# Kernel tuning notes

Measured on AMD Instinct MI355X. Metric: run time of the kernel, lower is better.

Reference implementation:

```python
import jax, jax.numpy as jnp
import numpy as np

DT, TAU_S, TAU_M = 1.0, 4.0, 20.0
ALPHA = float(np.exp(-DT / TAU_S))   # synaptic current decay
BETA = float(np.exp(-DT / TAU_M))    # membrane potential decay
THRESH = 1.0
STEPS, BATCH, D1, D2 = 128, 256, 1024, 1024


def setup_inputs() -> dict:
    key = jax.random.key(0)
    k1, k2 = jax.random.split(key)
    inp = jax.random.uniform(k1, (STEPS, BATCH, D1), dtype=jnp.float32)
    # kaiming_normal_ on (d2, d1): std = sqrt(2 / fan_in), mu = 1.0
    weight = jax.random.normal(k2, (D2, D1), dtype=jnp.float32) * np.sqrt(2.0 / D1)
    return {"input": inp, "weight": weight}


def reference(input, weight):
    steps, batch = input.shape[0], input.shape[1]
    d2 = weight.shape[0]
    # Step i uses input[i-1]; precompute all linear projections at once.
    lin = jnp.einsum('tbi,oi->tbo', input[:-1], weight)  # [steps-1, B, d2]

    def step(carry, cur):
        syn, mem = carry
        # snntorch Synaptic, reset_mechanism='zero': reset from PREVIOUS mem
        reset = (mem > THRESH).astype(mem.dtype)
        syn = ALPHA * syn + cur
        mem = (BETA * mem + syn) * (1.0 - reset)
        spk = (mem > THRESH).astype(mem.dtype)
        return (syn, mem), (spk, mem, syn)

    init = (jnp.zeros((batch, d2), input.dtype), jnp.zeros((batch, d2), input.dtype))
    _, (spk, V, I) = jax.lax.scan(step, init, lin)
    z = jnp.zeros((1, batch, d2), input.dtype)  # step 0 stays zero
    output = jnp.concatenate([z, spk], axis=0)
    V = jnp.concatenate([z, V], axis=0)
    I = jnp.concatenate([z, I], axis=0)
    return output, V, I
```

## Files before the change

kernel.cpp:

```cpp
#include <hip/hip_runtime.h>
#include <hip/hip_fp16.h>


#define STEPS 128
#define BATCH 256
#define DIN   1024
#define DOUT  1024

#define ALPHA 0.7788007830714049f
#define BETA  0.9512294245007140f

constexpr int    GM      = (STEPS - 1) * BATCH;
constexpr size_t PLANE   = (size_t)BATCH * DOUT;
constexpr size_t W_ELEMS = (size_t)DOUT * DIN;

typedef __attribute__((ext_vector_type(8))) _Float16 half8;
typedef __attribute__((ext_vector_type(4))) float float4v;

__global__ __launch_bounds__(256)
void split_kernel(const float* __restrict__ x,
                  unsigned short* __restrict__ hi,
                  unsigned short* __restrict__ lo)
{
    const size_t i = (size_t)blockIdx.x * 256 + threadIdx.x;
    const float4 v = reinterpret_cast<const float4*>(x)[i];
    float f[4] = {v.x, v.y, v.z, v.w};
    unsigned short hb[4], lb[4];
#pragma unroll
    for (int j = 0; j < 4; ++j) {
        _Float16 h = (_Float16)f[j];
        _Float16 l = (_Float16)(f[j] - (float)h);
        hb[j] = *reinterpret_cast<unsigned short*>(&h);
        lb[j] = *reinterpret_cast<unsigned short*>(&l);
    }
    ushort4 hv = {hb[0], hb[1], hb[2], hb[3]};
    ushort4 lv = {lb[0], lb[1], lb[2], lb[3]};
    reinterpret_cast<ushort4*>(hi)[i] = hv;
    reinterpret_cast<ushort4*>(lo)[i] = lv;
}

__device__ __forceinline__ void load16(const unsigned short* g, unsigned short* l)
{
    __builtin_amdgcn_global_load_lds(
        (const __attribute__((address_space(1))) void*)g,
        (__attribute__((address_space(3))) void*)l, 16, 0, 0);
}

__device__ __forceinline__ half8 ldsr(unsigned addr)
{
    half8 r;
    asm volatile("ds_read_b128 %0, %1" : "=v"(r) : "v"(addr) : "memory");
    return r;
}

#define PHASE_PRE() do {                                        \
    __builtin_amdgcn_s_barrier();                               \
    asm volatile("s_waitcnt lgkmcnt(0)" ::: "memory");          \
    __builtin_amdgcn_sched_barrier(0);                          \
    __builtin_amdgcn_s_setprio(1);                              \
} while (0)

#define PHASE_POST() do {                                       \
    __builtin_amdgcn_s_setprio(0);                              \
    __builtin_amdgcn_sched_barrier(0);                          \
    __builtin_amdgcn_s_barrier();                               \
} while (0)

#define MFMA_BLK(MB, BV)                                        \
    _Pragma("unroll")                                           \
    for (int mm = 0; mm < 4; ++mm)                              \
        _Pragma("unroll")                                       \
        for (int nn = 0; nn < 4; ++nn)                          \
            acc[(MB) + mm][nn] = __builtin_amdgcn_mfma_f32_16x16x32_f16( \
                ah[(MB) + mm], BV[nn], acc[(MB) + mm][nn], 0, 0, 0)

__global__ __launch_bounds__(512, 2)
void gemm_kernel(const float* __restrict__ Af,
                 const unsigned short* __restrict__ Wh,
                 const unsigned short* __restrict__ Wl,
                 float* __restrict__ C)
{
    __shared__ __align__(16) unsigned short smem[65536];

    const int lin = blockIdx.x;
    const int xcd = lin & 7, slot = lin >> 3;
    const int mp  = xcd * 16 + (slot >> 2);
    const int nt  = slot & 3;
    if (mp >= GM / 256) return;
    const int m0 = mp * 256;
    const int n0 = nt * 256;

    const int t = threadIdx.x;
    const int w = t >> 6, l = t & 63;
    const int wr = w >> 2, wc = w & 3;
    const int lr = l & 15, q = l >> 4;

    const int swz = q ^ ((l >> 1) & 3);

    const unsigned rdA = (unsigned)((wr * 128 + lr) * 64 + swz * 16);
    const unsigned rdB = (unsigned)(32768 + (wc * 64 + lr) * 64 + swz * 16);

    const int srow = l >> 2;
    const int sgE  = ((l & 3) ^ ((l >> 3) & 3)) * 8;

    const size_t fA0 = (size_t)(m0 + w * 32 +      srow) * DIN + sgE;
    const size_t fA1 = (size_t)(m0 + w * 32 + 16 + srow) * DIN + sgE;
    const size_t sB0 = (size_t)(n0 + w * 32 +      srow) * DIN + sgE;
    const size_t sB1 = (size_t)(n0 + w * 32 + 16 + srow) * DIN + sgE;

    const unsigned dstA = (unsigned)(w * 1024 + l * 8);

    auto STAGE_W = [&](int ks) {
        const int kk = (ks & 31) << 5;
        unsigned short* d = smem + ((ks & 1) << 15) + w * 1024;
        load16(Wh + sB0 + kk, d + 16384);
        load16(Wh + sB1 + kk, d + 16896);
        load16(Wl + sB0 + kk, d + 24576);
        load16(Wl + sB1 + kk, d + 25088);
    };

    auto WRITE_A = [&](float4 x, float4 y, unsigned short* ds, unsigned off) {
        float f[8] = {x.x, x.y, x.z, x.w, y.x, y.y, y.z, y.w};
        half8 h, lo8;
#pragma unroll
        for (int j = 0; j < 8; ++j) {
            _Float16 hh = (_Float16)f[j];
            h[j]   = hh;
            lo8[j] = (_Float16)(f[j] - (float)hh);
        }
        *reinterpret_cast<half8*>(ds + dstA + off)        = h;
        *reinterpret_cast<half8*>(ds + dstA + off + 8192) = lo8;
    };

    float4v acc[8][4];
#pragma unroll
    for (int m = 0; m < 8; ++m)
#pragma unroll
        for (int n = 0; n < 4; ++n)
            acc[m][n] = (float4v){0.f, 0.f, 0.f, 0.f};

    {
        float4 a0 = *reinterpret_cast<const float4*>(Af + fA0);
        float4 a1 = *reinterpret_cast<const float4*>(Af + fA0 + 4);
        float4 a2 = *reinterpret_cast<const float4*>(Af + fA1);
        float4 a3 = *reinterpret_cast<const float4*>(Af + fA1 + 4);
        STAGE_W(0);
        unsigned short* ds = smem;
        WRITE_A(a0, a1, ds, 0);
        WRITE_A(a2, a3, ds, 512);
        asm volatile("s_waitcnt vmcnt(0) lgkmcnt(0)" ::: "memory");
        __builtin_amdgcn_s_barrier();
    }

    for (int kt = 0; kt < 32; ++kt) {
        const unsigned sb = (unsigned)((kt & 1) << 16);
        const int kn = ((kt + 1) & 31) << 5;
        half8 ah[8], bh[4], bl[4];

        float4 a0 = *reinterpret_cast<const float4*>(Af + fA0 + kn);
        float4 a1 = *reinterpret_cast<const float4*>(Af + fA0 + kn + 4);
        float4 a2 = *reinterpret_cast<const float4*>(Af + fA1 + kn);
        float4 a3 = *reinterpret_cast<const float4*>(Af + fA1 + kn + 4);
#pragma unroll
        for (int m = 0; m < 4; ++m) ah[m] = ldsr(sb + rdA + m * 1024);
#pragma unroll
        for (int n = 0; n < 4; ++n) bh[n] = ldsr(sb + rdB + n * 1024);
        PHASE_PRE();  MFMA_BLK(0, bh);  PHASE_POST();

#pragma unroll
        for (int m = 4; m < 8; ++m) ah[m] = ldsr(sb + rdA + m * 1024);
        PHASE_PRE();  MFMA_BLK(4, bh);  PHASE_POST();

#pragma unroll
        for (int n = 0; n < 4; ++n) bl[n] = ldsr(sb + rdB + 16384 + n * 1024);
        STAGE_W((kt + 1) & 31);
        PHASE_PRE();  MFMA_BLK(0, bl);  PHASE_POST();

#pragma unroll
        for (int m = 0; m < 4; ++m) ah[m] = ldsr(sb + rdA + 16384 + m * 1024);
        PHASE_PRE();  MFMA_BLK(4, bl);  PHASE_POST();

#pragma unroll
        for (int m = 4; m < 8; ++m) ah[m] = ldsr(sb + rdA + 16384 + m * 1024);
        PHASE_PRE();  MFMA_BLK(0, bh);  PHASE_POST();

        PHASE_PRE();  MFMA_BLK(4, bh);
        __builtin_amdgcn_s_setprio(0);
        __builtin_amdgcn_sched_barrier(0);
        {
            unsigned short* ds = smem + (((kt + 1) & 1) << 15);
            WRITE_A(a0, a1, ds, 0);
            WRITE_A(a2, a3, ds, 512);
        }
        asm volatile("s_waitcnt vmcnt(0) lgkmcnt(0)" ::: "memory");
        __builtin_amdgcn_s_barrier();
    }

    const int mw = m0 + wr * 128 + q * 4;
    const int nw = n0 + wc * 64 + lr;
#pragma unroll
    for (int m = 0; m < 8; ++m)
#pragma unroll
        for (int n = 0; n < 4; ++n)
#pragma unroll
            for (int rg = 0; rg < 4; ++rg)
                C[(size_t)(mw + m * 16 + rg) * DOUT + (nw + n * 16)] = acc[m][n][rg];
}

__global__ __launch_bounds__(256)
void scan_kernel(float* __restrict__ out)
{
    const int idx = blockIdx.x * 256 + threadIdx.x;
    float* o0 = out;
    float* o1 = out + STEPS * PLANE;
    float* o2 = out + 2 * STEPS * PLANE;

    __builtin_nontemporal_store(0.0f, &o0[idx]);
    __builtin_nontemporal_store(0.0f, &o1[idx]);
    __builtin_nontemporal_store(0.0f, &o2[idx]);

    float n1 = o2[idx + PLANE];
    float n2 = o2[idx + 2 * PLANE];
    float n3 = o2[idx + 3 * PLANE];

    float syn = 0.0f, mem = 0.0f;
    size_t off = idx;
    for (int i = 1; i < STEPS; ++i) {
        off += PLANE;
        const float cur = n1; n1 = n2; n2 = n3;
        if (i + 3 < STEPS) n3 = o2[off + 3 * PLANE];
        const float reset = (mem > 1.0f) ? 1.0f : 0.0f;
        syn = ALPHA * syn + cur;
        mem = (BETA * mem + syn) * (1.0f - reset);
        const float spk = (mem > 1.0f) ? 1.0f : 0.0f;
        __builtin_nontemporal_store(spk, &o0[off]);
        __builtin_nontemporal_store(mem, &o1[off]);
        __builtin_nontemporal_store(syn, &o2[off]);
    }
}

extern "C" void kernel_launch(void* const* d_in, const int* in_sizes, int n_in,
                              void* d_out, int out_size, void* d_ws, size_t ws_size,
                              hipStream_t stream)
{
    const float* input  = (const float*)d_in[0];
    const float* weight = (const float*)d_in[1];
    float* out = (float*)d_out;

    unsigned short* Wh = (unsigned short*)(out + STEPS * PLANE);
    unsigned short* Wl = Wh + W_ELEMS;
    float* lin = out + 2 * STEPS * PLANE + PLANE;

    split_kernel<<<(int)(W_ELEMS / 1024), 256, 0, stream>>>(weight, Wh, Wl);

    gemm_kernel<<<512, 512, 0, stream>>>(input, Wh, Wl, lin);

    scan_kernel<<<(int)(PLANE / 256), 256, 0, stream>>>(out);
}
```

Before: 629.7 us.

## Switch GEMM to 32x32x16 MFMA tiles and vectorize scan to float2

The GEMM inner loop now uses 32x32x16 f16 MFMA instructions instead of 16x16x32. That needs new LDS read addressing with XOR swizzle groups, 4x2 accumulator fragments of 16 floats, and a new epilogue store mapping. Larger MFMA tiles mean fewer instructions and fewer LDS operand reads per FLOP. The scan kernel now handles two neurons per thread with float2 loads and stores and launches half as many blocks, which widens memory transactions but lowers thread-level parallelism.

```diff
diff --git a/kernel.cpp b/kernel.cpp
--- a/kernel.cpp
+++ b/kernel.cpp
@@ -14,8 +14,9 @@
 constexpr size_t PLANE   = (size_t)BATCH * DOUT;
 constexpr size_t W_ELEMS = (size_t)DOUT * DIN;
 
-typedef __attribute__((ext_vector_type(8))) _Float16 half8;
-typedef __attribute__((ext_vector_type(4))) float float4v;
+typedef __attribute__((ext_vector_type(8)))  _Float16 half8;
+typedef __attribute__((ext_vector_type(16))) float    f32x16;
+typedef __attribute__((ext_vector_type(2)))  float    f32x2;
 
 __global__ __launch_bounds__(256)
 void split_kernel(const float* __restrict__ x,
@@ -66,13 +67,13 @@
     __builtin_amdgcn_s_barrier();                               \
 } while (0)
 
-#define MFMA_BLK(MB, BV)                                        \
+#define MFMA8(AARR, AO, BARR, BO)                               \
     _Pragma("unroll")                                           \
-    for (int mm = 0; mm < 4; ++mm)                              \
+    for (int fm = 0; fm < 4; ++fm)                              \
         _Pragma("unroll")                                       \
-        for (int nn = 0; nn < 4; ++nn)                          \
-            acc[(MB) + mm][nn] = __builtin_amdgcn_mfma_f32_16x16x32_f16( \
-                ah[(MB) + mm], BV[nn], acc[(MB) + mm][nn], 0, 0, 0)
+        for (int fn = 0; fn < 2; ++fn)                          \
+            acc[fm][fn] = __builtin_amdgcn_mfma_f32_32x32x16_f16( \
+                AARR[(AO) + fm], BARR[(BO) + fn], acc[fm][fn], 0, 0, 0)
 
 __global__ __launch_bounds__(512, 2)
 void gemm_kernel(const float* __restrict__ Af,
@@ -93,12 +94,13 @@
     const int t = threadIdx.x;
     const int w = t >> 6, l = t & 63;
     const int wr = w >> 2, wc = w & 3;
-    const int lr = l & 15, q = l >> 4;
-
-    const int swz = q ^ ((l >> 1) & 3);
-
-    const unsigned rdA = (unsigned)((wr * 128 + lr) * 64 + swz * 16);
-    const unsigned rdB = (unsigned)(32768 + (wc * 64 + lr) * 64 + swz * 16);
+
+    const unsigned xorb = (unsigned)(((l >> 1) & 3) * 16);
+    const unsigned g0b  = ((unsigned)((l >> 5) * 16)) ^ xorb;
+    const unsigned g1b  = ((unsigned)((2 + (l >> 5)) * 16)) ^ xorb;
+
+    const unsigned rdA  = (unsigned)((wr * 128 + (l & 31)) * 64);
+    const unsigned rdB  = (unsigned)(32768 + (wc * 64 + (l & 31)) * 64);
 
     const int srow = l >> 2;
     const int sgE  = ((l & 3) ^ ((l >> 3) & 3)) * 8;
@@ -132,12 +134,14 @@
         *reinterpret_cast<half8*>(ds + dstA + off + 8192) = lo8;
     };
 
-    float4v acc[8][4];
-#pragma unroll
-    for (int m = 0; m < 8; ++m)
-#pragma unroll
-        for (int n = 0; n < 4; ++n)
-            acc[m][n] = (float4v){0.f, 0.f, 0.f, 0.f};
+    f32x16 acc[4][2];
+#pragma unroll
+    for (int fm = 0; fm < 4; ++fm)
+#pragma unroll
+        for (int fn = 0; fn < 2; ++fn)
+#pragma unroll
+            for (int rg = 0; rg < 16; ++rg)
+                acc[fm][fn][rg] = 0.f;
 
     {
         float4 a0 = *reinterpret_cast<const float4*>(Af + fA0);
@@ -155,36 +159,42 @@
     for (int kt = 0; kt < 32; ++kt) {
         const unsigned sb = (unsigned)((kt & 1) << 16);
         const int kn = ((kt + 1) & 31) << 5;
-        half8 ah[8], bh[4], bl[4];
+        half8 ahi[8], alo[8], bhi[4], blo[4];
 
         float4 a0 = *reinterpret_cast<const float4*>(Af + fA0 + kn);
         float4 a1 = *reinterpret_cast<const float4*>(Af + fA0 + kn + 4);
         float4 a2 = *reinterpret_cast<const float4*>(Af + fA1 + kn);
         float4 a3 = *reinterpret_cast<const float4*>(Af + fA1 + kn + 4);
 #pragma unroll
-        for (int m = 0; m < 4; ++m) ah[m] = ldsr(sb + rdA + m * 1024);
-#pragma unroll
-        for (int n = 0; n < 4; ++n) bh[n] = ldsr(sb + rdB + n * 1024);
-        PHASE_PRE();  MFMA_BLK(0, bh);  PHASE_POST();
-
-#pragma unroll
-        for (int m = 4; m < 8; ++m) ah[m] = ldsr(sb + rdA + m * 1024);
-        PHASE_PRE();  MFMA_BLK(4, bh);  PHASE_POST();
-
-#pragma unroll
-        for (int n = 0; n < 4; ++n) bl[n] = ldsr(sb + rdB + 16384 + n * 1024);
+        for (int fm = 0; fm < 4; ++fm) ahi[fm] = ldsr(sb + rdA + fm * 2048 + g0b);
+#pragma unroll
+        for (int fn = 0; fn < 2; ++fn) {
+            bhi[fn]     = ldsr(sb + rdB + fn * 2048 + g0b);
+            bhi[2 + fn] = ldsr(sb + rdB + fn * 2048 + g1b);
+        }
+        PHASE_PRE();  MFMA8(ahi, 0, bhi, 0);  PHASE_POST();
+
+#pragma unroll
+        for (int fm = 0; fm < 4; ++fm) ahi[4 + fm] = ldsr(sb + rdA + fm * 2048 + g1b);
+        PHASE_PRE();  MFMA8(ahi, 4, bhi, 2);  PHASE_POST();
+
+#pragma unroll
+        for (int fn = 0; fn < 2; ++fn) {
+            blo[fn]     = ldsr(sb + rdB + 16384 + fn * 2048 + g0b);
+            blo[2 + fn] = ldsr(sb + rdB + 16384 + fn * 2048 + g1b);
+        }
         STAGE_W((kt + 1) & 31);
-        PHASE_PRE();  MFMA_BLK(0, bl);  PHASE_POST();
-
-#pragma unroll
-        for (int m = 0; m < 4; ++m) ah[m] = ldsr(sb + rdA + 16384 + m * 1024);
-        PHASE_PRE();  MFMA_BLK(4, bl);  PHASE_POST();
-
-#pragma unroll
-        for (int m = 4; m < 8; ++m) ah[m] = ldsr(sb + rdA + 16384 + m * 1024);
-        PHASE_PRE();  MFMA_BLK(0, bh);  PHASE_POST();
-
-        PHASE_PRE();  MFMA_BLK(4, bh);
+        PHASE_PRE();  MFMA8(ahi, 0, blo, 0);  PHASE_POST();
+
+#pragma unroll
+        for (int fm = 0; fm < 4; ++fm) alo[fm] = ldsr(sb + rdA + 16384 + fm * 2048 + g0b);
+        PHASE_PRE();  MFMA8(ahi, 4, blo, 2);  PHASE_POST();
+
+#pragma unroll
+        for (int fm = 0; fm < 4; ++fm) alo[4 + fm] = ldsr(sb + rdA + 16384 + fm * 2048 + g1b);
+        PHASE_PRE();  MFMA8(alo, 0, bhi, 0);  PHASE_POST();
+
+        PHASE_PRE();  MFMA8(alo, 4, bhi, 2);
         __builtin_amdgcn_s_setprio(0);
         __builtin_amdgcn_sched_barrier(0);
         {
@@ -196,43 +206,50 @@
         __builtin_amdgcn_s_barrier();
     }
 
-    const int mw = m0 + wr * 128 + q * 4;
-    const int nw = n0 + wc * 64 + lr;
-#pragma unroll
-    for (int m = 0; m < 8; ++m)
-#pragma unroll
-        for (int n = 0; n < 4; ++n)
-#pragma unroll
-            for (int rg = 0; rg < 4; ++rg)
-                C[(size_t)(mw + m * 16 + rg) * DOUT + (nw + n * 16)] = acc[m][n][rg];
+    const int mwb = m0 + wr * 128 + ((l >> 5) << 2);
+    const int nwb = n0 + wc * 64 + (l & 31);
+#pragma unroll
+    for (int fm = 0; fm < 4; ++fm)
+#pragma unroll
+        for (int fn = 0; fn < 2; ++fn)
+#pragma unroll
+            for (int rg = 0; rg < 16; ++rg)
+                C[(size_t)(mwb + fm * 32 + (rg & 3) + ((rg >> 2) << 3)) * DOUT
+                  + nwb + fn * 32] = acc[fm][fn][rg];
 }
 
 __global__ __launch_bounds__(256)
 void scan_kernel(float* __restrict__ out)
 {
     const int idx = blockIdx.x * 256 + threadIdx.x;
-    float* o0 = out;
-    float* o1 = out + STEPS * PLANE;
-    float* o2 = out + 2 * STEPS * PLANE;
-
-    __builtin_nontemporal_store(0.0f, &o0[idx]);
-    __builtin_nontemporal_store(0.0f, &o1[idx]);
-    __builtin_nontemporal_store(0.0f, &o2[idx]);
-
-    float n1 = o2[idx + PLANE];
-    float n2 = o2[idx + 2 * PLANE];
-    float n3 = o2[idx + 3 * PLANE];
-
-    float syn = 0.0f, mem = 0.0f;
+    constexpr int P2 = (int)(PLANE / 2);
+    f32x2* o0 = reinterpret_cast<f32x2*>(out);
+    f32x2* o1 = reinterpret_cast<f32x2*>(out + STEPS * PLANE);
+    f32x2* o2 = reinterpret_cast<f32x2*>(out + 2 * STEPS * PLANE);
+
+    const f32x2 z = {0.f, 0.f};
+    __builtin_nontemporal_store(z, &o0[idx]);
+    __builtin_nontemporal_store(z, &o1[idx]);
+    __builtin_nontemporal_store(z, &o2[idx]);
+
+    f32x2 n1 = o2[idx + P2];
+    f32x2 n2 = o2[idx + 2 * P2];
+    f32x2 n3 = o2[idx + 3 * P2];
+
+    f32x2 syn = z, mem = z;
     size_t off = idx;
     for (int i = 1; i < STEPS; ++i) {
-        off += PLANE;
-        const float cur = n1; n1 = n2; n2 = n3;
-        if (i + 3 < STEPS) n3 = o2[off + 3 * PLANE];
-        const float reset = (mem > 1.0f) ? 1.0f : 0.0f;
+        off += P2;
+        const f32x2 cur = n1; n1 = n2; n2 = n3;
+        if (i + 3 < STEPS) n3 = o2[off + 3 * P2];
+        f32x2 reset;
+        reset.x = (mem.x > 1.0f) ? 1.0f : 0.0f;
+        reset.y = (mem.y > 1.0f) ? 1.0f : 0.0f;
         syn = ALPHA * syn + cur;
         mem = (BETA * mem + syn) * (1.0f - reset);
-        const float spk = (mem > 1.0f) ? 1.0f : 0.0f;
+        f32x2 spk;
+        spk.x = (mem.x > 1.0f) ? 1.0f : 0.0f;
+        spk.y = (mem.y > 1.0f) ? 1.0f : 0.0f;
         __builtin_nontemporal_store(spk, &o0[off]);
         __builtin_nontemporal_store(mem, &o1[off]);
         __builtin_nontemporal_store(syn, &o2[off]);
@@ -255,5 +272,5 @@
 
     gemm_kernel<<<512, 512, 0, stream>>>(input, Wh, Wl, lin);
 
-    scan_kernel<<<(int)(PLANE / 256), 256, 0, stream>>>(out);
-}
+    scan_kernel<<<(int)(PLANE / 512), 256, 0, stream>>>(out);
+}
```

New measurement: 645.0 us. +2.4%, slower.
